# Performance work log

Measured on AMD Instinct MI355X. Metric: run time of the kernel, lower is better.

The kernel has to match this reference:

```python
import jax, jax.numpy as jnp
import numpy as np

N = 100_000      # nodes
E = 400_000      # edges
POS = 3          # pos_dim
F = 128          # feats_dim (kernel_dim)
M = 16           # m_dim
FE = 16          # fourier_features
EIN = 2 * F + 2 * FE + 1   # 289 edge mlp input
EHID = 2 * EIN             # 578
NIN = F + M                # 144
NHID = 2 * F               # 256
EPS = 1e-5


def _ln(x, g, b):
    m = x.mean(-1, keepdims=True)
    v = ((x - m) ** 2).mean(-1, keepdims=True)
    return (x - m) * jax.lax.rsqrt(v + EPS) * g + b


def setup_inputs() -> dict:
    key = jax.random.key(0)
    ks = jax.random.split(key, 8)

    def xav(k, i, o):
        return jax.random.normal(k, (i, o), jnp.float32) * np.float32(np.sqrt(2.0 / (i + o)))

    x = jax.random.normal(ks[0], (N, POS + F), jnp.float32)
    edge_index = jax.random.randint(ks[1], (2, E), 0, N, dtype=jnp.int64)
    return {
        "x": x,
        "edge_index": edge_index,
        "e_w1": xav(ks[2], EIN, EHID), "e_b1": jnp.zeros((EHID,), jnp.float32),
        "e_w2": xav(ks[3], EHID, M),   "e_b2": jnp.zeros((M,), jnp.float32),
        "en1_g": jnp.ones((M,), jnp.float32), "en1_b": jnp.zeros((M,), jnp.float32),
        "en2_g": jnp.ones((M,), jnp.float32), "en2_b": jnp.zeros((M,), jnp.float32),
        "nn1_g": jnp.ones((F,), jnp.float32), "nn1_b": jnp.zeros((F,), jnp.float32),
        "n_w1": xav(ks[4], NIN, NHID), "n_b1": jnp.zeros((NHID,), jnp.float32),
        "n_w2": xav(ks[5], NHID, F),   "n_b2": jnp.zeros((F,), jnp.float32),
        "nn2_g": jnp.ones((F,), jnp.float32), "nn2_b": jnp.zeros((F,), jnp.float32),
    }


def reference(x, edge_index, e_w1, e_b1, e_w2, e_b2, en1_g, en1_b, en2_g, en2_b,
              nn1_g, nn1_b, n_w1, n_b1, n_w2, n_b2, nn2_g, nn2_b):
    coors, feats = x[:, :POS], x[:, POS:]
    src, dst = edge_index[0], edge_index[1]  # x_j = feats[src], x_i = feats[dst]

    rel = coors[src] - coors[dst]                      # [E,3]
    d = (rel ** 2).sum(-1, keepdims=True)              # [E,1] squared distance
    scales = jnp.asarray(2.0, jnp.float32) ** jnp.arange(FE)
    ds = d / scales                                    # [E,FE]
    edge_attr = jnp.concatenate([jnp.sin(ds), jnp.cos(ds), d], -1)  # [E,2*FE+1]

    # edge MLP + LayerNorm (message)
    m = jnp.concatenate([feats[dst], feats[src], edge_attr], -1)    # [E,EIN]
    m = jax.nn.silu(m @ e_w1 + e_b1)
    m = jax.nn.silu(m @ e_w2 + e_b2)                                # [E,M]
    m = _ln(m, en1_g, en1_b)

    # scatter-add to target nodes, then LayerNorm
    m_i = jax.ops.segment_sum(m, dst, num_segments=N)               # [N,M]
    m_i = _ln(m_i, en2_g, en2_b)

    # node update MLP with residual
    h = jnp.concatenate([_ln(feats, nn1_g, nn1_b), m_i], -1)        # [N,NIN]
    h = jax.nn.silu(h @ n_w1 + n_b1)
    h = h @ n_w2 + n_b2
    h = _ln(h, nn2_g, nn2_b)
    out = feats + h
    return jnp.concatenate([coors, out], -1)                        # [N,POS+F]
```

## Files before the change

### kernel.cpp

```cpp
#include <hip/hip_runtime.h>
#include <math.h>

#define N_NODES 100000
#define N_EDGES 400000
#define POSD 3
#define F 128
#define M 16
#define EIN 289
#define EHID 578
#define NIN 144
#define NHID 256
#define ROW 131
#define LNEPS 1e-5f

#define KP 320
#define KPA 328
#define NP 640
#define EPB 32
#define NSLICE 10
#define NTW 5
#define HIDP 640
#define HIDPA 648

#define NPB2 80
#define NK1P 168
#define NSL2 5
#define NHIDP 264

#define PSTR 584
#define ARBF_STR 72

#define WS_W1KS   6400000
#define WS_W2T    6809600
#define WS_FEATS  6830080
#define WS_W1KS2  32430080
#define WS_W2KS   32512000
#define WS_B1H    32577536
#define WS_PD     33554432LL
#define WS_PS     (WS_PD + 116800000LL + 4096LL)
#define WS_FAST_NEED (WS_PS + 116800000LL + 4096LL)

typedef _Float16 half8 __attribute__((ext_vector_type(8)));
typedef _Float16 half4 __attribute__((ext_vector_type(4)));
typedef float f32x4 __attribute__((ext_vector_type(4)));

__device__ __forceinline__ float silu_f(float v) {
    return v * __builtin_amdgcn_rcpf(1.f + __expf(-v));
}

__global__ __launch_bounds__(256) void prep_feats(
    const float* __restrict__ x, _Float16* __restrict__ feats)
{
    long long i = (long long)blockIdx.x * 256 + threadIdx.x;
    if (i < (long long)N_NODES * F) {
        int n = (int)(i >> 7), k = (int)(i & 127);
        feats[i] = (_Float16)x[(long long)n * ROW + POSD + k];
    }
}

__global__ __launch_bounds__(256) void prep_weights(
    const float* __restrict__ w1, const float* __restrict__ w2,
    const float* __restrict__ b1,
    _Float16* __restrict__ w1ks, _Float16* __restrict__ w2t,
    _Float16* __restrict__ b1h)
{
    long long idx = (long long)blockIdx.x * 256 + threadIdx.x;
    const long long n1 = (long long)NSLICE * NP * 32;
    const long long n2 = n1 + (long long)M * HIDP;
    if (idx < n1) {
        int s   = (int)(idx / (NP * 32));
        int rem = (int)(idx - (long long)s * (NP * 32));
        int c   = rem >> 5;
        int kk  = rem & 31;
        int k   = s * 32 + kk;
        float v = (k < EIN && c < EHID) ? w1[(long long)k * EHID + c] : 0.f;
        w1ks[idx] = (_Float16)v;
    } else if (idx < n2) {
        long long j = idx - n1;
        int oc = (int)(j / HIDP);
        int k  = (int)(j - (long long)oc * HIDP);
        float v = (k < EHID) ? w2[(long long)k * M + oc] : 0.f;
        w2t[j] = (_Float16)v;
    } else if (idx < n2 + HIDP) {
        int j = (int)(idx - n2);
        b1h[j] = (_Float16)((j < EHID) ? b1[j] : 0.f);
    }
}

__global__ __launch_bounds__(256) void prep_weights_node(
    const float* __restrict__ w1, const float* __restrict__ w2,
    _Float16* __restrict__ w1ks2, _Float16* __restrict__ w2ks)
{
    int idx = blockIdx.x * 256 + threadIdx.x;
    const int n1 = NSL2 * 256 * 32;
    if (idx < n1) {
        int s = idx >> 13, rem = idx & 8191;
        int c = rem >> 5, kk = rem & 31;
        int k = s * 32 + kk;
        w1ks2[idx] = (_Float16)((k < NIN) ? w1[k * NHID + c] : 0.f);
    } else if (idx < n1 + 8 * 128 * 32) {
        int j = idx - n1;
        int s = j >> 12, rem = j & 4095;
        int c = rem >> 5, kk = rem & 31;
        int k = s * 32 + kk;
        w2ks[j] = (_Float16)w2[k * F + c];
    }
}

__global__ __launch_bounds__(512, 2) void prep_pdps(
    const _Float16* __restrict__ feats, const _Float16* __restrict__ w1ks,
    _Float16* __restrict__ Pd, _Float16* __restrict__ Ps)
{
    const int t = threadIdx.x;
    const int lane = t & 63, wv = t >> 6, cl16 = lane & 15, h4 = lane >> 4;
    const long long nb = (long long)blockIdx.x * NPB2;
    const bool live[5] = {
        (wv * 5 + 0) * 16 < EHID, (wv * 5 + 1) * 16 < EHID,
        (wv * 5 + 2) * 16 < EHID, (wv * 5 + 3) * 16 < EHID,
        (wv * 5 + 4) * 16 < EHID };

    #pragma unroll
    for (int hf = 0; hf < 2; ++hf) {
        _Float16* P = hf ? Ps : Pd;
        f32x4 acc[5][5] = {};
        #pragma unroll
        for (int s = 0; s < 4; ++s) {
            half8 bf[5];
            #pragma unroll
            for (int nt = 0; nt < 5; ++nt)
                if (live[nt])
                    bf[nt] = *(const half8*)(w1ks + (long long)(hf * 4 + s) * (NP * 32)
                                             + (wv * 5 + nt) * 512 + cl16 * 32 + h4 * 8);
            half8 af[5];
            #pragma unroll
            for (int mt = 0; mt < 5; ++mt)
                af[mt] = *(const half8*)(feats + (nb + mt * 16 + cl16) * F + s * 32 + h4 * 8);
            #pragma unroll
            for (int nt = 0; nt < 5; ++nt)
                if (live[nt]) {
                    #pragma unroll
                    for (int mt = 0; mt < 5; ++mt)
                        acc[mt][nt] = __builtin_amdgcn_mfma_f32_16x16x32_f16(
                                          af[mt], bf[nt], acc[mt][nt], 0, 0, 0);
                }
        }
        #pragma unroll
        for (int nt = 0; nt < 5; ++nt) {
            if (!live[nt]) continue;
            int hcol = (wv * 5 + nt) * 16 + cl16;
            if (hcol < PSTR) {
                #pragma unroll
                for (int mt = 0; mt < 5; ++mt) {
                    #pragma unroll
                    for (int r = 0; r < 4; ++r) {
                        int row = mt * 16 + h4 * 4 + r;
                        P[(nb + row) * PSTR + hcol] = (_Float16)acc[mt][nt][r];
                    }
                }
            }
        }
    }
}

__global__ __launch_bounds__(512, 4) void edge_fast(
    const float* __restrict__ x, const int* __restrict__ ei,
    const _Float16* __restrict__ w1ks, const _Float16* __restrict__ b1h,
    const _Float16* __restrict__ w2t, const float* __restrict__ b2,
    const float* __restrict__ g1, const float* __restrict__ bb1,
    float* __restrict__ m_i,
    const _Float16* __restrict__ Pd, const _Float16* __restrict__ Ps)
{
    __shared__ __align__(16) _Float16 lds_H[EPB * HIDPA];
    __shared__ __align__(16) char ubuf[8192];
    __shared__ int   src_s[EPB], dst_s[EPB];
    __shared__ float d_s[EPB];
    _Float16* A_rbf = (_Float16*)ubuf;
    float (*part)[EPB][M] = (float (*)[EPB][M])ubuf;

    const int t    = threadIdx.x;
    const int lane = t & 63;
    const int wv   = t >> 6;
    const int cl16 = lane & 15;
    const int h4   = lane >> 4;
    const long long ebase = (long long)blockIdx.x * EPB;

    if (t < EPB) {
        int s = ei[ebase + t];
        int d = ei[(long long)N_EDGES + ebase + t];
        src_s[t] = s; dst_s[t] = d;
        float dx = x[(long long)s*ROW+0] - x[(long long)d*ROW+0];
        float dy = x[(long long)s*ROW+1] - x[(long long)d*ROW+1];
        float dz = x[(long long)s*ROW+2] - x[(long long)d*ROW+2];
        d_s[t] = dx*dx + dy*dy + dz*dz;
    }
    __syncthreads();

    for (int i = t; i < EPB * 64; i += 512) {
        int row = i >> 6, j = i & 63;
        float dv = d_s[row];
        float ds = ldexpf(dv, -(j & 15));
        float v = (j < 16) ? __sinf(ds) : (j < 32) ? __cosf(ds)
                : (j == 32) ? dv : 0.f;
        A_rbf[row * ARBF_STR + j] = (_Float16)v;
    }
    __syncthreads();

    f32x4 acc[2][NTW] = {};
    const bool live[NTW] = {
        (wv * NTW + 0) * 16 < EHID, (wv * NTW + 1) * 16 < EHID,
        (wv * NTW + 2) * 16 < EHID, (wv * NTW + 3) * 16 < EHID,
        (wv * NTW + 4) * 16 < EHID };
    #pragma unroll
    for (int s = 0; s < 2; ++s) {
        half8 bf[NTW];
        #pragma unroll
        for (int nt = 0; nt < NTW; ++nt)
            if (live[nt])
                bf[nt] = *(const half8*)(w1ks + (long long)(8 + s) * (NP * 32)
                                         + (wv * NTW + nt) * 512 + cl16 * 32 + h4 * 8);
        #pragma unroll
        for (int mt = 0; mt < 2; ++mt) {
            const half8 af = *(const half8*)(A_rbf + (mt * 16 + cl16) * ARBF_STR
                                             + s * 32 + h4 * 8);
            #pragma unroll
            for (int nt = 0; nt < NTW; ++nt)
                if (live[nt])
                    acc[mt][nt] = __builtin_amdgcn_mfma_f32_16x16x32_f16(
                                      af, bf[nt], acc[mt][nt], 0, 0, 0);
        }
    }

    half8 bq[5];
    {
        const int kq = wv >> 1;
        #pragma unroll
        for (int k5 = 0; k5 < 5; ++k5)
            bq[k5] = *(const half8*)(w2t + cl16 * HIDP + (kq * 5 + k5) * 32 + h4 * 8);
    }
    half8 pd8[5], ps8[5];
    #pragma unroll
    for (int p = 0; p < 5; ++p) {
        int i5 = t + p * 512;
        int e  = i5 / 80;
        int g  = i5 - e * 80;
        pd8[p] = *(const half8*)(Pd + (long long)dst_s[e] * PSTR + g * 8);
        ps8[p] = *(const half8*)(Ps + (long long)src_s[e] * PSTR + g * 8);
    }

    #pragma unroll
    for (int nt = 0; nt < NTW; ++nt) {
        if (!live[nt]) continue;
        int hcol = (wv * NTW + nt) * 16 + cl16;
        #pragma unroll
        for (int mt = 0; mt < 2; ++mt) {
            #pragma unroll
            for (int r = 0; r < 4; ++r) {
                int edge = mt * 16 + h4 * 4 + r;
                lds_H[edge * HIDPA + hcol] = (_Float16)acc[mt][nt][r];
            }
        }
    }
    __syncthreads();

    #pragma unroll
    for (int p = 0; p < 5; ++p) {
        int i5 = t + p * 512;
        int e  = i5 / 80;
        int g  = i5 - e * 80;
        half8 rb = *(const half8*)(lds_H + e * HIDPA + g * 8);
        half8 bb = *(const half8*)(b1h + g * 8);
        half8 o;
        #pragma unroll
        for (int j = 0; j < 8; ++j) {
            int h = g * 8 + j;
            float v = (float)pd8[p][j] + (float)ps8[p][j]
                    + (float)rb[j] + (float)bb[j];
            o[j] = (h < EHID) ? (_Float16)silu_f(v) : (_Float16)0.f;
        }
        *(half8*)(lds_H + e * HIDPA + g * 8) = o;
    }
    __syncthreads();

    {
        const int eh = wv & 1;
        const int kq = wv >> 1;
        f32x4 acc2 = {};
        const int oc = cl16;
        const int edgeA = eh * 16 + oc;
        #pragma unroll
        for (int k5 = 0; k5 < 5; ++k5) {
            int G2 = (kq * 5 + k5) * 4 + h4;
            const half8 a = *(const half8*)(lds_H + edgeA * HIDPA + G2 * 8);
            acc2 = __builtin_amdgcn_mfma_f32_16x16x32_f16(a, bq[k5], acc2, 0, 0, 0);
        }
        #pragma unroll
        for (int r = 0; r < 4; ++r)
            part[kq][eh * 16 + h4 * 4 + r][cl16] = acc2[r];
    }
    __syncthreads();

    if (wv < 2) {
        const int eh = wv;
        const int oc = cl16;
        float g = g1[oc], bb = bb1[oc], b2v = b2[oc];
        #pragma unroll
        for (int r = 0; r < 4; ++r) {
            int edge = eh * 16 + h4 * 4 + r;
            float v = part[0][edge][oc] + part[1][edge][oc]
                    + part[2][edge][oc] + part[3][edge][oc] + b2v;
            v = silu_f(v);
            float s = v, s2 = v * v;
            #pragma unroll
            for (int m = 8; m >= 1; m >>= 1) {
                s  += __shfl_xor(s,  m, 16);
                s2 += __shfl_xor(s2, m, 16);
            }
            float mean = s * (1.f / 16.f);
            float var  = s2 * (1.f / 16.f) - mean * mean;
            float outv = (v - mean) * rsqrtf(var + LNEPS) * g + bb;
            atomicAdd(&m_i[(long long)dst_s[edge] * M + oc], outv);
        }
    }
}

__global__ __launch_bounds__(512, 4) void edge_fused(
    const _Float16* __restrict__ feats, const float* __restrict__ x,
    const int* __restrict__ ei,
    const _Float16* __restrict__ w1ks, const float* __restrict__ b1,
    const _Float16* __restrict__ w2t, const float* __restrict__ b2,
    const float* __restrict__ g1, const float* __restrict__ bb1,
    float* __restrict__ m_i)
{
    __shared__ __align__(16) _Float16 smem[EPB * HIDPA];
    _Float16* lds_A = smem;
    _Float16* lds_H = smem;
    __shared__ float part[4][EPB][M];
    __shared__ int   src_s[EPB], dst_s[EPB];
    __shared__ float d_s[EPB];

    const int t    = threadIdx.x;
    const int lane = t & 63;
    const int wv   = t >> 6;
    const int cl16 = lane & 15;
    const int h4   = lane >> 4;
    const long long ebase = (long long)blockIdx.x * EPB;

    if (t < EPB) {
        int s = ei[ebase + t];
        int d = ei[(long long)N_EDGES + ebase + t];
        src_s[t] = s; dst_s[t] = d;
        float dx = x[(long long)s*ROW+0] - x[(long long)d*ROW+0];
        float dy = x[(long long)s*ROW+1] - x[(long long)d*ROW+1];
        float dz = x[(long long)s*ROW+2] - x[(long long)d*ROW+2];
        d_s[t] = dx*dx + dy*dy + dz*dz;
    }
    __syncthreads();

    for (int i = t; i < EPB * 32; i += 512) {
        int row = i >> 5, g = i & 31;
        int node = (g < 16) ? dst_s[row] : src_s[row];
        half8 v = *(const half8*)(feats + (long long)node * F + ((g & 15) << 3));
        *(half8*)(lds_A + row * KPA + (g << 3)) = v;
    }
    for (int i = t; i < EPB * 64; i += 512) {
        int row = i >> 6, j = i & 63;
        float dv = d_s[row];
        float ds = ldexpf(dv, -(j & 15));
        float v = (j < 16) ? __sinf(ds) : (j < 32) ? __cosf(ds)
                : (j == 32) ? dv : 0.f;
        lds_A[row * KPA + 256 + j] = (_Float16)v;
    }
    __syncthreads();

    f32x4 acc[2][NTW] = {};
    const bool live[NTW] = {
        (wv * NTW + 0) * 16 < EHID, (wv * NTW + 1) * 16 < EHID,
        (wv * NTW + 2) * 16 < EHID, (wv * NTW + 3) * 16 < EHID,
        (wv * NTW + 4) * 16 < EHID };
    #pragma unroll
    for (int s = 0; s < NSLICE; ++s) {
        half8 bf[NTW];
        #pragma unroll
        for (int nt = 0; nt < NTW; ++nt)
            if (live[nt])
                bf[nt] = *(const half8*)(w1ks + (long long)s * (NP * 32)
                                         + (wv * NTW + nt) * 512 + cl16 * 32 + h4 * 8);
        const int G = s * 4 + h4;
        half8 af[2];
        #pragma unroll
        for (int mt = 0; mt < 2; ++mt)
            af[mt] = *(const half8*)(lds_A + (mt * 16 + cl16) * KPA + G * 8);
        #pragma unroll
        for (int nt = 0; nt < NTW; ++nt)
            if (live[nt]) {
                #pragma unroll
                for (int mt = 0; mt < 2; ++mt)
                    acc[mt][nt] = __builtin_amdgcn_mfma_f32_16x16x32_f16(
                                      af[mt], bf[nt], acc[mt][nt], 0, 0, 0);
            }
    }

    half8 bq[5];
    {
        const int kq = wv >> 1;
        #pragma unroll
        for (int k5 = 0; k5 < 5; ++k5)
            bq[k5] = *(const half8*)(w2t + cl16 * HIDP + (kq * 5 + k5) * 32 + h4 * 8);
    }
    __syncthreads();

    #pragma unroll
    for (int nt = 0; nt < NTW; ++nt) {
        int hcol = (wv * NTW + nt) * 16 + cl16;
        float bias = (hcol < EHID) ? b1[hcol] : 0.f;
        #pragma unroll
        for (int mt = 0; mt < 2; ++mt) {
            #pragma unroll
            for (int r = 0; r < 4; ++r) {
                int edge = mt * 16 + h4 * 4 + r;
                float v = (hcol < EHID) ? silu_f(acc[mt][nt][r] + bias) : 0.f;
                lds_H[edge * HIDPA + hcol] = (_Float16)v;
            }
        }
    }
    __syncthreads();

    {
        const int eh = wv & 1;
        const int kq = wv >> 1;
        f32x4 acc2 = {};
        const int oc = cl16;
        const int edgeA = eh * 16 + oc;
        #pragma unroll
        for (int k5 = 0; k5 < 5; ++k5) {
            int G2 = (kq * 5 + k5) * 4 + h4;
            const half8 a = *(const half8*)(lds_H + edgeA * HIDPA + G2 * 8);
            acc2 = __builtin_amdgcn_mfma_f32_16x16x32_f16(a, bq[k5], acc2, 0, 0, 0);
        }
        #pragma unroll
        for (int r = 0; r < 4; ++r)
            part[kq][eh * 16 + h4 * 4 + r][oc] = acc2[r];
    }
    __syncthreads();

    if (wv < 2) {
        const int eh = wv;
        const int oc = cl16;
        float g = g1[oc], bb = bb1[oc], b2v = b2[oc];
        #pragma unroll
        for (int r = 0; r < 4; ++r) {
            int edge = eh * 16 + h4 * 4 + r;
            float v = part[0][edge][oc] + part[1][edge][oc]
                    + part[2][edge][oc] + part[3][edge][oc] + b2v;
            v = silu_f(v);
            float s = v, s2 = v * v;
            #pragma unroll
            for (int m = 8; m >= 1; m >>= 1) {
                s  += __shfl_xor(s,  m, 16);
                s2 += __shfl_xor(s2, m, 16);
            }
            float mean = s * (1.f / 16.f);
            float var  = s2 * (1.f / 16.f) - mean * mean;
            float outv = (v - mean) * rsqrtf(var + LNEPS) * g + bb;
            atomicAdd(&m_i[(long long)dst_s[edge] * M + oc], outv);
        }
    }
}

__global__ __launch_bounds__(512, 4) void node_kernel(
    const _Float16* __restrict__ feats, const float* __restrict__ x,
    const float* __restrict__ m_i,
    const float* __restrict__ en2g, const float* __restrict__ en2b,
    const float* __restrict__ nn1g, const float* __restrict__ nn1b,
    const _Float16* __restrict__ w1ks2, const float* __restrict__ b1,
    const _Float16* __restrict__ w2ks, const float* __restrict__ b2,
    const float* __restrict__ nn2g, const float* __restrict__ nn2b,
    float* __restrict__ out)
{
    __shared__ __align__(16) _Float16 smem[NPB2 * NHIDP];
    _Float16* lds_A = smem;
    _Float16* lds_H = smem;
    __shared__ float rsum2[NPB2], rsq2[NPB2];

    const int t    = threadIdx.x;
    const int lane = t & 63;
    const int wv   = t >> 6;
    const int cl16 = lane & 15;
    const int h4   = lane >> 4;
    const long long nb = (long long)blockIdx.x * NPB2;

    if (t < NPB2) { rsum2[t] = 0.f; rsq2[t] = 0.f; }

    #pragma unroll
    for (int p = 0; p < 5; ++p) {
        int nl = p * 16 + (t >> 5);
        int l  = t & 31;
        half4 v4 = *(const half4*)(feats + (nb + nl) * F + l * 4);
        float v[4]; float s = 0.f, s2 = 0.f;
        #pragma unroll
        for (int i = 0; i < 4; ++i) {
            v[i] = (float)v4[i]; s += v[i]; s2 += v[i]*v[i];
        }
        #pragma unroll
        for (int m = 16; m >= 1; m >>= 1) {
            s  += __shfl_xor(s,  m, 32);
            s2 += __shfl_xor(s2, m, 32);
        }
        float mean = s * (1.f/128.f);
        float var  = s2 * (1.f/128.f) - mean*mean;
        float rs   = rsqrtf(var + LNEPS);
        half4 w;
        #pragma unroll
        for (int i = 0; i < 4; ++i) {
            int c = l * 4 + i;
            w[i] = (_Float16)((v[i] - mean) * rs * nn1g[c] + nn1b[c]);
        }
        *(half4*)(lds_A + nl * NK1P + l * 4) = w;
    }
    for (int i = t; i < NPB2 * M; i += 512) {
        int nl = i >> 4, oc = i & 15;
        float v = m_i[(nb + nl) * M + oc];
        float a = v, a2 = v * v;
        #pragma unroll
        for (int m = 8; m >= 1; m >>= 1) {
            a  += __shfl_xor(a,  m, 16);
            a2 += __shfl_xor(a2, m, 16);
        }
        float mn = a * (1.f/16.f);
        float vr = a2 * (1.f/16.f) - mn*mn;
        float lv = (v - mn) * rsqrtf(vr + LNEPS) * en2g[oc] + en2b[oc];
        lds_A[nl * NK1P + 128 + oc] = (_Float16)lv;
    }
    for (int i = t; i < NPB2 * 16; i += 512) {
        int nl = i >> 4, j = i & 15;
        lds_A[nl * NK1P + 144 + j] = (_Float16)0.f;
    }
    __syncthreads();

    f32x4 acc[5][2] = {};
    #pragma unroll
    for (int s = 0; s < NSL2; ++s) {
        half8 bf[2];
        #pragma unroll
        for (int nt = 0; nt < 2; ++nt)
            bf[nt] = *(const half8*)(w1ks2 + s * (NHID * 32)
                                     + (wv * 2 + nt) * 512 + cl16 * 32 + h4 * 8);
        const int G = s * 4 + h4;
        half8 af[5];
        #pragma unroll
        for (int mt = 0; mt < 5; ++mt)
            af[mt] = *(const half8*)(lds_A + (mt * 16 + cl16) * NK1P + G * 8);
        #pragma unroll
        for (int nt = 0; nt < 2; ++nt) {
            #pragma unroll
            for (int mt = 0; mt < 5; ++mt)
                acc[mt][nt] = __builtin_amdgcn_mfma_f32_16x16x32_f16(
                                  af[mt], bf[nt], acc[mt][nt], 0, 0, 0);
        }
    }
    __syncthreads();

    #pragma unroll
    for (int nt = 0; nt < 2; ++nt) {
        int hcol = (wv * 2 + nt) * 16 + cl16;
        float bias = b1[hcol];
        #pragma unroll
        for (int mt = 0; mt < 5; ++mt) {
            #pragma unroll
            for (int r = 0; r < 4; ++r) {
                int row = mt * 16 + h4 * 4 + r;
                float v = silu_f(acc[mt][nt][r] + bias);
                lds_H[row * NHIDP + hcol] = (_Float16)v;
            }
        }
    }
    __syncthreads();

    f32x4 acc2[5] = {};
    const int col = wv * 16 + cl16;
    #pragma unroll
    for (int s = 0; s < 8; ++s) {
        const half8 b = *(const half8*)(w2ks + s * (F * 32) + col * 32 + h4 * 8);
        const int G2 = s * 4 + h4;
        #pragma unroll
        for (int mt = 0; mt < 5; ++mt) {
            int row = mt * 16 + cl16;
            const half8 a = *(const half8*)(lds_H + row * NHIDP + G2 * 8);
            acc2[mt] = __builtin_amdgcn_mfma_f32_16x16x32_f16(a, b, acc2[mt], 0, 0, 0);
        }
    }

    float y[5][4];
    float b2v = b2[col];
    #pragma unroll
    for (int mt = 0; mt < 5; ++mt) {
        #pragma unroll
        for (int r = 0; r < 4; ++r) {
            float v = acc2[mt][r] + b2v;
            y[mt][r] = v;
            float s = v, s2 = v * v;
            #pragma unroll
            for (int m = 8; m >= 1; m >>= 1) {
                s  += __shfl_xor(s,  m, 16);
                s2 += __shfl_xor(s2, m, 16);
            }
            if (cl16 == 0) {
                int row = mt * 16 + h4 * 4 + r;
                atomicAdd(&rsum2[row], s);
                atomicAdd(&rsq2[row],  s2);
            }
        }
    }
    __syncthreads();

    float gcol2 = nn2g[col], bcol2 = nn2b[col];
    #pragma unroll
    for (int mt = 0; mt < 5; ++mt) {
        #pragma unroll
        for (int r = 0; r < 4; ++r) {
            int row = mt * 16 + h4 * 4 + r;
            long long node = nb + row;
            float mn = rsum2[row] * (1.f/128.f);
            float vr = rsq2[row] * (1.f/128.f) - mn*mn;
            float rs = rsqrtf(vr + LNEPS);
            float res = x[node * ROW + POSD + col];
            out[node * ROW + POSD + col] = res + (y[mt][r] - mn) * rs * gcol2 + bcol2;
        }
    }
    for (int i = t; i < NPB2 * POSD; i += 512) {
        int nl = i / 3, c = i - nl * 3;
        long long node = nb + nl;
        out[node * ROW + c] = x[node * ROW + c];
    }
}

extern "C" void kernel_launch(void* const* d_in, const int* in_sizes, int n_in,
                              void* d_out, int out_size, void* d_ws, size_t ws_size,
                              hipStream_t stream) {
    const float* x    = (const float*)d_in[0];
    const int*   ei   = (const int*)d_in[1];
    const float* e_w1 = (const float*)d_in[2];
    const float* e_b1 = (const float*)d_in[3];
    const float* e_w2 = (const float*)d_in[4];
    const float* e_b2 = (const float*)d_in[5];
    const float* en1g = (const float*)d_in[6];
    const float* en1b = (const float*)d_in[7];
    const float* en2g = (const float*)d_in[8];
    const float* en2b = (const float*)d_in[9];
    const float* nn1g = (const float*)d_in[10];
    const float* nn1b = (const float*)d_in[11];
    const float* n_w1 = (const float*)d_in[12];
    const float* n_b1 = (const float*)d_in[13];
    const float* n_w2 = (const float*)d_in[14];
    const float* n_b2 = (const float*)d_in[15];
    const float* nn2g = (const float*)d_in[16];
    const float* nn2b = (const float*)d_in[17];
    float* out = (float*)d_out;

    char* ws = (char*)d_ws;
    float*    m_i   = (float*)ws;
    _Float16* w1ks  = (_Float16*)(ws + WS_W1KS);
    _Float16* w2t   = (_Float16*)(ws + WS_W2T);
    _Float16* feats = (_Float16*)(ws + WS_FEATS);
    _Float16* w1ks2 = (_Float16*)(ws + WS_W1KS2);
    _Float16* w2ks  = (_Float16*)(ws + WS_W2KS);
    _Float16* b1h   = (_Float16*)(ws + WS_B1H);
    _Float16* Pd    = (_Float16*)(ws + WS_PD);
    _Float16* Ps    = (_Float16*)(ws + WS_PS);

    const bool fast = ws_size >= (size_t)WS_FAST_NEED;

    hipMemsetAsync(m_i, 0, (size_t)N_NODES * M * sizeof(float), stream);
    prep_weights<<<843, 256, 0, stream>>>(e_w1, e_w2, e_b1, w1ks, w2t, b1h);
    prep_weights_node<<<288, 256, 0, stream>>>(n_w1, n_w2, w1ks2, w2ks);
    prep_feats<<<(N_NODES * F + 255) / 256, 256, 0, stream>>>(x, feats);

    if (fast) {
        prep_pdps<<<N_NODES / NPB2, 512, 0, stream>>>(feats, w1ks, Pd, Ps);
        edge_fast<<<N_EDGES / EPB, 512, 0, stream>>>(
            x, ei, w1ks, b1h, w2t, e_b2, en1g, en1b, m_i, Pd, Ps);
    } else {
        edge_fused<<<N_EDGES / EPB, 512, 0, stream>>>(
            feats, x, ei, w1ks, e_b1, w2t, e_b2, en1g, en1b, m_i);
    }
    node_kernel<<<N_NODES / NPB2, 512, 0, stream>>>(
        feats, x, m_i, en2g, en2b, nn1g, nn1b, w1ks2, n_b1, w2ks, n_b2, nn2g, nn2b, out);
}
```

Baseline: 543.6 us.

## Stage Pd/Ps stores through LDS, hoist gathers earlier, sum in fp16

In prep_pdps, MFMA accumulators are first staged into a shared tile and then written to global memory as coalesced half8 rows, replacing scattered 2-byte stores. In edge_fast, the Pd/Ps row gathers and the w2 fragment loads move ahead of the RBF/MFMA stage so their latency can overlap with that compute. The gather indexing is reorganised so 16 threads cover one edge row, which drops the divide-by-80. The four-term pre-activation sum is now done as packed fp16 vector adds instead of fp32, which lowers precision and adds extra __syncthreads in prep.

Result: slower. 560.4 us (+3.1%).

```diff
diff --git a/kernel.cpp b/kernel.cpp
--- a/kernel.cpp
+++ b/kernel.cpp
@@ -111,6 +111,7 @@
     const _Float16* __restrict__ feats, const _Float16* __restrict__ w1ks,
     _Float16* __restrict__ Pd, _Float16* __restrict__ Ps)
 {
+    __shared__ __align__(16) _Float16 st[32][PSTR];
     const int t = threadIdx.x;
     const int lane = t & 63, wv = t >> 6, cl16 = lane & 15, h4 = lane >> 4;
     const long long nb = (long long)blockIdx.x * NPB2;
@@ -121,7 +122,7 @@
 
     #pragma unroll
     for (int hf = 0; hf < 2; ++hf) {
-        _Float16* P = hf ? Ps : Pd;
+        _Float16* __restrict__ P = hf ? Ps : Pd;
         f32x4 acc[5][5] = {};
         #pragma unroll
         for (int s = 0; s < 4; ++s) {
@@ -145,16 +146,36 @@
                 }
         }
         #pragma unroll
-        for (int nt = 0; nt < 5; ++nt) {
-            if (!live[nt]) continue;
-            int hcol = (wv * 5 + nt) * 16 + cl16;
-            if (hcol < PSTR) {
+        for (int ch = 0; ch < 3; ++ch) {
+            const int nmt = (ch == 2) ? 1 : 2;
+            __syncthreads();
+            #pragma unroll
+            for (int mi = 0; mi < 2; ++mi) {
+                if (mi < nmt) {
+                    int mt = ch * 2 + mi;
+                    #pragma unroll
+                    for (int nt = 0; nt < 5; ++nt) {
+                        if (!live[nt]) continue;
+                        int hcol = (wv * 5 + nt) * 16 + cl16;
+                        if (hcol < PSTR) {
+                            #pragma unroll
+                            for (int r = 0; r < 4; ++r)
+                                st[mi * 16 + h4 * 4 + r][hcol] = (_Float16)acc[mt][nt][r];
+                        }
+                    }
+                }
+            }
+            __syncthreads();
+            const int nrow = nmt * 16;
+            const int row = t >> 4;
+            const int gw  = t & 15;
+            if (row < nrow) {
                 #pragma unroll
-                for (int mt = 0; mt < 5; ++mt) {
-                    #pragma unroll
-                    for (int r = 0; r < 4; ++r) {
-                        int row = mt * 16 + h4 * 4 + r;
-                        P[(nb + row) * PSTR + hcol] = (_Float16)acc[mt][nt][r];
+                for (int k = 0; k < 5; ++k) {
+                    int g = gw + 16 * k;
+                    if (g < PSTR / 8) {
+                        *(half8*)(P + (nb + ch * 32 + row) * PSTR + g * 8)
+                            = *(const half8*)(&st[row][g * 8]);
                     }
                 }
             }
@@ -195,6 +216,25 @@
     }
     __syncthreads();
 
+    const int ce = t >> 4;
+    const int g0 = t & 15;
+    const long long pdrow = (long long)dst_s[ce] * PSTR;
+    const long long psrow = (long long)src_s[ce] * PSTR;
+    half8 pd8[5], ps8[5];
+    #pragma unroll
+    for (int p = 0; p < 5; ++p) {
+        int g = g0 + 16 * p;
+        pd8[p] = *(const half8*)(Pd + pdrow + g * 8);
+        ps8[p] = *(const half8*)(Ps + psrow + g * 8);
+    }
+    half8 bq[5];
+    {
+        const int kq = wv >> 1;
+        #pragma unroll
+        for (int k5 = 0; k5 < 5; ++k5)
+            bq[k5] = *(const half8*)(w2t + cl16 * HIDP + (kq * 5 + k5) * 32 + h4 * 8);
+    }
+
     for (int i = t; i < EPB * 64; i += 512) {
         int row = i >> 6, j = i & 63;
         float dv = d_s[row];
@@ -230,23 +270,6 @@
         }
     }
 
-    half8 bq[5];
-    {
-        const int kq = wv >> 1;
-        #pragma unroll
-        for (int k5 = 0; k5 < 5; ++k5)
-            bq[k5] = *(const half8*)(w2t + cl16 * HIDP + (kq * 5 + k5) * 32 + h4 * 8);
-    }
-    half8 pd8[5], ps8[5];
-    #pragma unroll
-    for (int p = 0; p < 5; ++p) {
-        int i5 = t + p * 512;
-        int e  = i5 / 80;
-        int g  = i5 - e * 80;
-        pd8[p] = *(const half8*)(Pd + (long long)dst_s[e] * PSTR + g * 8);
-        ps8[p] = *(const half8*)(Ps + (long long)src_s[e] * PSTR + g * 8);
-    }
-
     #pragma unroll
     for (int nt = 0; nt < NTW; ++nt) {
         if (!live[nt]) continue;
@@ -264,20 +287,18 @@
 
     #pragma unroll
     for (int p = 0; p < 5; ++p) {
-        int i5 = t + p * 512;
-        int e  = i5 / 80;
-        int g  = i5 - e * 80;
-        half8 rb = *(const half8*)(lds_H + e * HIDPA + g * 8);
+        int g = g0 + 16 * p;
+        half8 rb = *(const half8*)(lds_H + ce * HIDPA + g * 8);
         half8 bb = *(const half8*)(b1h + g * 8);
+        half8 sum = pd8[p] + ps8[p] + rb + bb;
         half8 o;
         #pragma unroll
         for (int j = 0; j < 8; ++j) {
             int h = g * 8 + j;
-            float v = (float)pd8[p][j] + (float)ps8[p][j]
-                    + (float)rb[j] + (float)bb[j];
+            float v = (float)sum[j];
             o[j] = (h < EHID) ? (_Float16)silu_f(v) : (_Float16)0.f;
         }
-        *(half8*)(lds_H + e * HIDPA + g * 8) = o;
+        *(half8*)(lds_H + ce * HIDPA + g * 8) = o;
     }
     __syncthreads();
 
```
